# Kernel tuning notes

Hardware: AMD Instinct MI355X
Metric: run time of the kernel (lower is better)

The kernel has to match this reference:

```python
import jax, jax.numpy as jnp
import numpy as np

E, B, S, D, F = 8, 2, 1024, 1024, 4096


def setup_inputs() -> dict:
    key = jax.random.key(0)
    ks = jax.random.split(key, 9)
    sc_d = 1.0 / np.sqrt(D)
    sc_f = 1.0 / np.sqrt(F)
    hidden_states = jax.random.normal(ks[0], (B, S, D), dtype=jnp.float32)
    # router outputs set externally on the parent model in the original code
    gating_probs = jax.nn.softmax(jax.random.normal(ks[1], (B, E), dtype=jnp.float32), axis=-1)
    shared_gate_prob = jax.nn.sigmoid(jax.random.normal(ks[2], (B, 1), dtype=jnp.float32))
    # stacked expert SwiGLU MLP weights (Llama-style gate/up/down)
    Wg = jax.random.normal(ks[3], (E, D, F), dtype=jnp.float32) * sc_d
    Wu = jax.random.normal(ks[4], (E, D, F), dtype=jnp.float32) * sc_d
    Wd = jax.random.normal(ks[5], (E, F, D), dtype=jnp.float32) * sc_f
    # shared expert MLP
    Sg = jax.random.normal(ks[6], (D, F), dtype=jnp.float32) * sc_d
    Su = jax.random.normal(ks[7], (D, F), dtype=jnp.float32) * sc_d
    Sd = jax.random.normal(ks[8], (F, D), dtype=jnp.float32) * sc_f
    return {
        "hidden_states": hidden_states,
        "gating_probs": gating_probs,
        "shared_gate_prob": shared_gate_prob,
        "Wg": Wg, "Wu": Wu, "Wd": Wd,
        "Sg": Sg, "Su": Su, "Sd": Sd,
    }


def reference(hidden_states, gating_probs, shared_gate_prob, Wg, Wu, Wd, Sg, Su, Sd):
    h = hidden_states  # [B,S,D]
    # every expert's MLP runs on all tokens (naive all-experts-dense, as in source)
    g = jnp.einsum("bsd,edf->ebsf", h, Wg)
    u = jnp.einsum("bsd,edf->ebsf", h, Wu)
    expert_outs = jnp.einsum("ebsf,efd->ebsd", jax.nn.silu(g) * u, Wd)  # [E,B,S,D]
    # weighted_sum routing with per-sequence gating probs [B,E]
    expert_output = jnp.einsum("be,ebsd->bsd", gating_probs, expert_outs)
    # shared expert MLP
    shared = jnp.einsum("bsf,fd->bsd", jax.nn.silu(h @ Sg) * (h @ Su), Sd)
    sg = shared_gate_prob[:, :, None]  # [B,1,1]
    return (1.0 - sg) * expert_output + sg * shared
```

## Files before the change

kernel.cpp:

```cpp
#include <hip/hip_runtime.h>
#include <cstdio>
#include <cstdint>

typedef _Float16 f16;
typedef _Float16 f16x4 __attribute__((ext_vector_type(4)));
typedef _Float16 f16x8 __attribute__((ext_vector_type(8)));
typedef float f32x4 __attribute__((ext_vector_type(4)));

#define GLL16(gp, lp)                                                          \
  __builtin_amdgcn_global_load_lds(                                            \
      (const __attribute__((address_space(1))) void*)(gp),                     \
      (__attribute__((address_space(3))) void*)(lp), 16, 0, 0)

__global__ void cvt_f32_f16_kernel(const float* __restrict__ in,
                                   f16* __restrict__ out, int n4) {
  int i = blockIdx.x * blockDim.x + threadIdx.x;
  if (i < n4) {
    f32x4 v = reinterpret_cast<const f32x4*>(in)[i];
    f16x4 o;
    o[0] = (f16)v[0]; o[1] = (f16)v[1]; o[2] = (f16)v[2]; o[3] = (f16)v[3];
    reinterpret_cast<f16x4*>(out)[i] = o;
  }
}

__global__ void tr_cvt2_kernel(const float* __restrict__ inA,
                               const float* __restrict__ inB,
                               f16* __restrict__ out, size_t slotOff,
                               int C, size_t OS, int nA) {
  int slot = blockIdx.z;
  const float* src = (slot < nA) ? inA + (size_t)slot * 64 * gridDim.y * C : inB;
  f16* dst = out + (size_t)slot * slotOff;
  __shared__ f16 tl[4096];
  int t = threadIdx.x;
  int r0 = blockIdx.y * 64, c0 = blockIdx.x * 64;
  int br = (t >> 4) * 4, bc = (t & 15) * 4;
  f32x4 v[4];
#pragma unroll
  for (int i = 0; i < 4; ++i)
    v[i] = *(const f32x4*)&src[(size_t)(r0 + br + i) * C + c0 + bc];
#pragma unroll
  for (int cc = 0; cc < 4; ++cc) {
    int c = bc + cc;
    f16x4 o;
    o[0] = (f16)v[0][cc]; o[1] = (f16)v[1][cc];
    o[2] = (f16)v[2][cc]; o[3] = (f16)v[3][cc];
    *(f16x4*)&tl[c * 64 + (br ^ ((c & 7) * 8))] = o;
  }
  __syncthreads();
  int rw = (t & 7) * 8, cw = t >> 3;
#pragma unroll
  for (int j = 0; j < 2; ++j) {
    int c = cw + j * 32;
    f16x8 o = *(const f16x8*)&tl[c * 64 + (rw ^ ((c & 7) * 8))];
    *(f16x8*)&dst[(size_t)(c0 + c) * OS + r0 + rw] = o;
  }
}

#define BARX __builtin_amdgcn_s_barrier()
#define WAITV4 { asm volatile("s_waitcnt vmcnt(4)" ::: "memory"); __builtin_amdgcn_sched_barrier(0); }
#define WAITV0 { asm volatile("s_waitcnt vmcnt(0)" ::: "memory"); __builtin_amdgcn_sched_barrier(0); }
#define WAITL0 { asm volatile("s_waitcnt lgkmcnt(0)" ::: "memory"); __builtin_amdgcn_sched_barrier(0); }

#define STAGE_A(tile, hf)                                                      \
  do {                                                                         \
    const f16* g_ = Abase + (size_t)((hf) * 128) * LD + (tile) * 64 + aVoff;   \
    f16* d_ = &lds[(2 * ((tile) & 1) + (hf)) * 8192 + w * 512];                \
    GLL16(g_, d_);                                                             \
    GLL16(g_ + (size_t)64 * LD, d_ + 4096);                                    \
  } while (0)
#define STAGE_B(tile, hf)                                                      \
  do {                                                                         \
    const f16* g_ = Bbase + (size_t)((hf) * 128) * LD + (tile) * 64 + aVoff;   \
    f16* d_ = &lds[32768 + (2 * ((tile) & 1) + (hf)) * 8192 + w * 512];        \
    GLL16(g_, d_);                                                             \
    GLL16(g_ + (size_t)64 * LD, d_ + 4096);                                    \
  } while (0)

#define RD_A(rh, buf)                                                          \
  do {                                                                         \
    const f16* p_ = &lds[(2 * (buf) + wr) * 8192 + (rh) * 4096];               \
    aF[0][0] = *(const f16x8*)(p_ + 0 * 1024 + vR0);                           \
    aF[0][1] = *(const f16x8*)(p_ + 0 * 1024 + vR1);                           \
    aF[1][0] = *(const f16x8*)(p_ + 1 * 1024 + vR0);                           \
    aF[1][1] = *(const f16x8*)(p_ + 1 * 1024 + vR1);                           \
    aF[2][0] = *(const f16x8*)(p_ + 2 * 1024 + vR0);                           \
    aF[2][1] = *(const f16x8*)(p_ + 2 * 1024 + vR1);                           \
    aF[3][0] = *(const f16x8*)(p_ + 3 * 1024 + vR0);                           \
    aF[3][1] = *(const f16x8*)(p_ + 3 * 1024 + vR1);                           \
  } while (0)
#define RD_B(ch, buf)                                                          \
  do {                                                                         \
    const f16* p_ = &lds[32768 + (2 * (buf) + bh) * 8192 + bq * 4096 +         \
                         (ch) * 2 * 1024];                                     \
    bF[(ch) * 2][0] = *(const f16x8*)(p_ + vR0);                               \
    bF[(ch) * 2][1] = *(const f16x8*)(p_ + vR1);                               \
    bF[(ch) * 2 + 1][0] = *(const f16x8*)(p_ + 1024 + vR0);                    \
    bF[(ch) * 2 + 1][1] = *(const f16x8*)(p_ + 1024 + vR1);                    \
  } while (0)

#define MFMA16(rh, ch)                                                         \
  do {                                                                         \
    __builtin_amdgcn_s_setprio(1);                                             \
    _Pragma("unroll") for (int rt = 0; rt < 4; ++rt)                           \
        _Pragma("unroll") for (int ct = 0; ct < 2; ++ct)                       \
        _Pragma("unroll") for (int ks = 0; ks < 2; ++ks)                       \
            acc[(rh) * 4 + rt][(ch) * 2 + ct] =                                \
        __builtin_amdgcn_mfma_f32_16x16x32_f16(                                \
            aF[rt][ks], bF[(ch) * 2 + ct][ks], acc[(rh) * 4 + rt][(ch) * 2 + ct], \
            0, 0, 0);                                                          \
    __builtin_amdgcn_s_setprio(0);                                             \
    __builtin_amdgcn_sched_barrier(0);                                         \
  } while (0)

template <int MODE>
__global__ __launch_bounds__(512, 2) void gemm256_kernel(
    const f16* __restrict__ A, const f16* __restrict__ B, f16* __restrict__ T,
    float* __restrict__ P, const float* __restrict__ gate,
    const float* __restrict__ sgp) {
  constexpr size_t LD = (MODE == 2) ? 36864 : 1024;
  constexpr int NTILES = (MODE == 2) ? 72 : 16;
  __shared__ __align__(16) f16 lds[65536];

  int mt, nt, slot, kpart;
  if (MODE == 2) {
    int wg = (blockIdx.x & 7) * 32 + (blockIdx.x >> 3);
    kpart = wg >> 5; mt = (wg >> 2) & 7; nt = wg & 3; slot = 0;
  } else {
    int wg = ((blockIdx.x & 7) * 144) + (blockIdx.x >> 3);
    mt = wg / 144;
    int r144 = wg % 144;
    slot = r144 >> 4; nt = r144 & 15; kpart = 0;
  }

  int t = threadIdx.x, w = t >> 6, l = t & 63;
  int wr = w >> 2, wc = w & 3;
  int bh = wc >> 1, bq = wc & 1;

  int scol = (((l & 7) ^ ((l >> 3) & 7)) * 8);
  size_t stRow = (size_t)(w * 8 + (l >> 3)) * LD;
  size_t aVoff = stRow + scol;
  const f16* Abase;
  const f16* Bbase;
  if (MODE == 2) {
    Abase = A + (size_t)mt * 256 * LD + (size_t)kpart * 4608;
    Bbase = B + (size_t)nt * 256 * LD + (size_t)kpart * 4608;
  } else {
    Abase = A + (size_t)mt * 256 * LD;
    Bbase = B + (size_t)slot * 4096 * 1024 + (size_t)nt * 256 * LD;
  }

  int vR0 = (l & 15) * 64 + (((l >> 4) * 8) ^ ((l & 7) * 8));
  int vR1 = (l & 15) * 64 + ((32 + (l >> 4) * 8) ^ ((l & 7) * 8));

  f16x8 aF[4][2], bF[4][2];
  f32x4 acc[8][4] = {};

  STAGE_B(0, 0); STAGE_B(0, 1);
  STAGE_A(0, 0); STAGE_A(0, 1);
  STAGE_B(1, 0); STAGE_B(1, 1);
  WAITV4;
  BARX;

#pragma unroll 1
  for (int it = 0; it < NTILES / 2 - 1; ++it) {
    int t1 = 2 * it + 1, t2 = 2 * it + 2, t3 = 2 * it + 3;
    RD_A(0, 0); RD_B(0, 0); STAGE_A(t1, 0);
    BARX; WAITL0; MFMA16(0, 0); BARX;
    RD_B(1, 0); STAGE_A(t1, 1);
    BARX; WAITL0; MFMA16(0, 1); BARX;
    RD_A(1, 0); STAGE_B(t2, 0);
    BARX; WAITL0; MFMA16(1, 0); BARX;
    STAGE_B(t2, 1);
    BARX; MFMA16(1, 1); WAITV4; BARX;
    RD_A(0, 1); RD_B(0, 1); STAGE_A(t2, 0);
    BARX; WAITL0; MFMA16(0, 0); BARX;
    RD_B(1, 1); STAGE_A(t2, 1);
    BARX; WAITL0; MFMA16(0, 1); BARX;
    RD_A(1, 1); STAGE_B(t3, 0);
    BARX; WAITL0; MFMA16(1, 0); BARX;
    STAGE_B(t3, 1);
    BARX; MFMA16(1, 1); WAITV4; BARX;
  }
  RD_A(0, 0); RD_B(0, 0); STAGE_A(NTILES - 1, 0);
  BARX; WAITL0; MFMA16(0, 0); BARX;
  RD_B(1, 0); STAGE_A(NTILES - 1, 1);
  BARX; WAITL0; MFMA16(0, 1); BARX;
  RD_A(1, 0);
  BARX; WAITL0; MFMA16(1, 0); BARX;
  BARX; MFMA16(1, 1); WAITV0; BARX;
  RD_A(0, 1); RD_B(0, 1);
  BARX; WAITL0; MFMA16(0, 0); BARX;
  RD_B(1, 1);
  BARX; WAITL0; MFMA16(0, 1); BARX;
  RD_A(1, 1);
  BARX; WAITL0; MFMA16(1, 0); BARX;
  MFMA16(1, 1);

  int r0 = (l >> 4) * 4, c0 = l & 15;
  if (MODE == 2) {
    size_t base = ((size_t)kpart << 21);
    int rowbase = mt * 256 + wr * 128;
    int colbase = nt * 256 + wc * 64;
#pragma unroll
    for (int rt = 0; rt < 8; ++rt)
#pragma unroll
      for (int ct = 0; ct < 4; ++ct)
#pragma unroll
        for (int j = 0; j < 4; ++j)
          P[base + (size_t)(rowbase + rt * 16 + r0 + j) * 1024 + colbase +
            ct * 16 + c0] = acc[rt][ct][j];
  } else {
    int rowbase = mt * 256 + wr * 128;
    size_t colbase = (size_t)slot * 4096 + nt * 256 + wc * 64;
    float coef = 0.f;
    if (MODE == 1) {
      int b = mt >> 2;
      float s = sgp[b];
      coef = (slot < 8) ? (1.f - s) * gate[b * 8 + slot] : s;
    }
#pragma unroll
    for (int rt = 0; rt < 8; ++rt) {
#pragma unroll
      for (int ct = 0; ct < 4; ++ct) {
#pragma unroll
        for (int j = 0; j < 4; ++j) {
          size_t idx = (size_t)(rowbase + rt * 16 + r0 + j) * 36864 + colbase +
                       ct * 16 + c0;
          float v = acc[rt][ct][j];
          if (MODE == 0) {
            T[idx] = (f16)v;
          } else {
            float u = (float)T[idx];
            T[idx] = (f16)(v / (1.f + __expf(-v)) * u * coef);
          }
        }
      }
    }
  }
}

__global__ void reduce8_kernel(const float* __restrict__ P,
                               float* __restrict__ out, int n4) {
  int i = blockIdx.x * blockDim.x + threadIdx.x;
  if (i < n4) {
    f32x4 s = {0.f, 0.f, 0.f, 0.f};
#pragma unroll
    for (int e = 0; e < 8; ++e) {
      f32x4 v = reinterpret_cast<const f32x4*>(P + ((size_t)e << 21))[i];
      s += v;
    }
    reinterpret_cast<f32x4*>(out)[i] = s;
  }
}

extern "C" void kernel_launch(void* const* d_in, const int* in_sizes, int n_in,
                              void* d_out, int out_size, void* d_ws,
                              size_t ws_size, hipStream_t stream) {
  const float* h    = (const float*)d_in[0];
  const float* gate = (const float*)d_in[1];
  const float* sgp  = (const float*)d_in[2];
  const float* Wg   = (const float*)d_in[3];
  const float* Wu   = (const float*)d_in[4];
  const float* Wd   = (const float*)d_in[5];
  const float* Sg   = (const float*)d_in[6];
  const float* Su   = (const float*)d_in[7];
  const float* Sd   = (const float*)d_in[8];

  const size_t SZ_HB = 4194304;
  const size_t SZ_W  = 75497472;
  const size_t SZ_T  = 150994944;
  const size_t SZ_P  = 67108864;
  char* ws = (char*)d_ws;
  f16*   hb  = (f16*)(ws);
  f16*   WgT = (f16*)(ws + SZ_HB);
  f16*   WuT = (f16*)(ws + SZ_HB + SZ_W);
  f16*   WdT = (f16*)(ws + SZ_HB + 2 * SZ_W);
  f16*   T   = (f16*)(ws + SZ_HB + 3 * SZ_W);
  float* P   = (float*)(ws + SZ_HB + 3 * SZ_W + SZ_T);
  size_t need = SZ_HB + 3 * SZ_W + SZ_T + SZ_P;
  if (ws_size < need) {
    fprintf(stderr, "kernel_launch: ws too small (%zu < %zu)\n", ws_size, need);
    return;
  }
  float* out = (float*)d_out;

  cvt_f32_f16_kernel<<<2048, 256, 0, stream>>>(h, hb, 524288);
  tr_cvt2_kernel<<<dim3(64, 16, 9), 256, 0, stream>>>(
      Wg, Sg, WgT, 4096ull * 1024, 4096, 1024, 8);
  tr_cvt2_kernel<<<dim3(64, 16, 9), 256, 0, stream>>>(
      Wu, Su, WuT, 4096ull * 1024, 4096, 1024, 8);
  tr_cvt2_kernel<<<dim3(16, 64, 9), 256, 0, stream>>>(
      Wd, Sd, WdT, 4096, 1024, 36864, 8);

  gemm256_kernel<0><<<1152, 512, 0, stream>>>(hb, WuT, T, nullptr, nullptr, nullptr);
  gemm256_kernel<1><<<1152, 512, 0, stream>>>(hb, WgT, T, nullptr, gate, sgp);
  gemm256_kernel<2><<<256, 512, 0, stream>>>(T, WdT, nullptr, P, nullptr, nullptr);
  reduce8_kernel<<<2048, 256, 0, stream>>>(P, out, 524288);
}
```

Before: 651.6 us.

## Fuse gate and up projections into one dual-accumulator GEMM kernel

Replaces the two separate up and gate GEMM launches, which wrote the up result to T and then read it back in the gate epilogue, with a single kernel. It stages A once per K tile along with both Wg and Wu tiles (256x128 output tile) and keeps two accumulator sets, applying SiLU(g)*u*coef in the epilogue. This avoids re-reading A and the f16 round trip of T. The cost is smaller N tiles and double the accumulator registers, which may reduce occupancy or MFMA efficiency.

```diff
diff --git a/kernel.cpp b/kernel.cpp
--- a/kernel.cpp
+++ b/kernel.cpp
@@ -11,6 +11,11 @@
   __builtin_amdgcn_global_load_lds(                                            \
       (const __attribute__((address_space(1))) void*)(gp),                     \
       (__attribute__((address_space(3))) void*)(lp), 16, 0, 0)
+
+#define BARX __builtin_amdgcn_s_barrier()
+#define WAITV4 { asm volatile("s_waitcnt vmcnt(4)" ::: "memory"); __builtin_amdgcn_sched_barrier(0); }
+#define WAITV0 { asm volatile("s_waitcnt vmcnt(0)" ::: "memory"); __builtin_amdgcn_sched_barrier(0); }
+#define WAITL0 { asm volatile("s_waitcnt lgkmcnt(0)" ::: "memory"); __builtin_amdgcn_sched_barrier(0); }
 
 __global__ void cvt_f32_f16_kernel(const float* __restrict__ in,
                                    f16* __restrict__ out, int n4) {
@@ -56,10 +61,135 @@
   }
 }
 
-#define BARX __builtin_amdgcn_s_barrier()
-#define WAITV4 { asm volatile("s_waitcnt vmcnt(4)" ::: "memory"); __builtin_amdgcn_sched_barrier(0); }
-#define WAITV0 { asm volatile("s_waitcnt vmcnt(0)" ::: "memory"); __builtin_amdgcn_sched_barrier(0); }
-#define WAITL0 { asm volatile("s_waitcnt lgkmcnt(0)" ::: "memory"); __builtin_amdgcn_sched_barrier(0); }
+#define STAGE_A3(NB)                                                           \
+  do {                                                                         \
+    f16* d_ = &lds[(NB) * 16384 + ldsT];                                       \
+    GLL16(aS, d_); GLL16(aS + 65536, d_ + 4096);                               \
+    GLL16(aS + 131072, d_ + 8192); GLL16(aS + 196608, d_ + 12288);             \
+  } while (0)
+#define STAGE_G3(NB)                                                           \
+  do {                                                                         \
+    f16* d_ = &lds[32768 + (NB) * 16384 + ldsT];                               \
+    GLL16(gS, d_); GLL16(gS + 65536, d_ + 4096);                               \
+  } while (0)
+#define STAGE_U3(NB)                                                           \
+  do {                                                                         \
+    f16* d_ = &lds[32768 + (NB) * 16384 + 8192 + ldsT];                        \
+    GLL16(uS, d_); GLL16(uS + 65536, d_ + 4096);                               \
+  } while (0)
+
+#define RD3(BUF, VK)                                                           \
+  do {                                                                         \
+    const f16* pa_ = &lds[(BUF) * 16384 + wr * 4096 + vRow + (VK)];            \
+    aF[0] = *(const f16x8*)(pa_);                                              \
+    aF[1] = *(const f16x8*)(pa_ + 1024);                                       \
+    aF[2] = *(const f16x8*)(pa_ + 2048);                                       \
+    aF[3] = *(const f16x8*)(pa_ + 3072);                                       \
+    const f16* pg_ = &lds[32768 + (BUF) * 16384 + wc * 4096 + vRow + (VK)];    \
+    bG[0] = *(const f16x8*)(pg_);                                              \
+    bG[1] = *(const f16x8*)(pg_ + 1024);                                       \
+    bG[2] = *(const f16x8*)(pg_ + 2048);                                       \
+    bG[3] = *(const f16x8*)(pg_ + 3072);                                       \
+    const f16* pu_ = pg_ + 8192;                                               \
+    bU[0] = *(const f16x8*)(pu_);                                              \
+    bU[1] = *(const f16x8*)(pu_ + 1024);                                       \
+    bU[2] = *(const f16x8*)(pu_ + 2048);                                       \
+    bU[3] = *(const f16x8*)(pu_ + 3072);                                       \
+  } while (0)
+
+#define MFMA32()                                                               \
+  do {                                                                         \
+    __builtin_amdgcn_s_setprio(1);                                             \
+    _Pragma("unroll") for (int mi = 0; mi < 4; ++mi)                           \
+        _Pragma("unroll") for (int ni = 0; ni < 4; ++ni) {                     \
+      ag[mi][ni] = __builtin_amdgcn_mfma_f32_16x16x32_f16(aF[mi], bG[ni],      \
+                                                          ag[mi][ni], 0, 0, 0);\
+      au[mi][ni] = __builtin_amdgcn_mfma_f32_16x16x32_f16(aF[mi], bU[ni],      \
+                                                          au[mi][ni], 0, 0, 0);\
+    }                                                                          \
+    __builtin_amdgcn_s_setprio(0);                                             \
+    __builtin_amdgcn_sched_barrier(0);                                         \
+  } while (0)
+
+#define BODY3(BUF, DOSTA, DOSTB)                                               \
+  do {                                                                         \
+    RD3(BUF, vK0);                                                             \
+    if (DOSTA) { STAGE_A3((BUF) ^ 1); }                                        \
+    BARX; WAITL0;                                                              \
+    MFMA32();                                                                  \
+    BARX;                                                                      \
+    RD3(BUF, vK1);                                                             \
+    if (DOSTB) {                                                               \
+      STAGE_G3((BUF) ^ 1); STAGE_U3((BUF) ^ 1);                                \
+      aS += 64; gS += 64; uS += 64;                                            \
+    }                                                                          \
+    BARX; WAITL0;                                                              \
+    MFMA32();                                                                  \
+    if (DOSTB) { WAITV0; }                                                     \
+    BARX;                                                                      \
+  } while (0)
+
+__global__ __launch_bounds__(512, 2) void gemmUG3_kernel(
+    const f16* __restrict__ A, const f16* __restrict__ Bg,
+    const f16* __restrict__ Bu, f16* __restrict__ T,
+    const float* __restrict__ gate, const float* __restrict__ sgp) {
+  __shared__ __align__(16) f16 lds[65536];
+
+  int lgl = (blockIdx.x & 7) * 288 + (blockIdx.x >> 3);
+  int mt = lgl & 7;
+  int ntg = lgl >> 3;
+  int slot = ntg >> 5;
+
+  int t = threadIdx.x, w = t >> 6, l = t & 63;
+  int wr = w >> 1, wc = w & 1;
+
+  int kqs = (((t & 7) ^ ((t >> 3) & 7)) * 8);
+  const f16* aS = A + (size_t)(mt * 256 + (t >> 3)) * 1024 + kqs;
+  const f16* gS = Bg + (size_t)slot * 4194304 +
+                  (size_t)((ntg & 31) * 128 + (t >> 3)) * 1024 + kqs;
+  const f16* uS = Bu + (size_t)slot * 4194304 +
+                  (size_t)((ntg & 31) * 128 + (t >> 3)) * 1024 + kqs;
+  int ldsT = t * 8;
+
+  int vRow = (l & 15) * 64;
+  int vK0 = (((l >> 4) ^ (l & 7))) * 8;
+  int vK1 = (((4 + (l >> 4)) ^ (l & 7))) * 8;
+
+  f16x8 aF[4], bG[4], bU[4];
+  f32x4 ag[4][4] = {}, au[4][4] = {};
+
+  STAGE_A3(0); STAGE_G3(0); STAGE_U3(0);
+  aS += 64; gS += 64; uS += 64;
+  WAITV0; BARX;
+
+#pragma unroll 1
+  for (int it = 0; it < 7; ++it) {
+    BODY3(0, 1, 1);
+    BODY3(1, 1, 1);
+  }
+  BODY3(0, 1, 1);
+  BODY3(1, 0, 0);
+
+  int r0 = (l >> 4) * 4, c0 = l & 15;
+  int rowb = mt * 256 + wr * 64;
+  size_t colb = (size_t)ntg * 128 + wc * 64;
+  int b = mt >> 2;
+  float s = sgp[b];
+  float coef = (slot < 8) ? (1.f - s) * gate[b * 8 + slot] : s;
+#pragma unroll
+  for (int mi = 0; mi < 4; ++mi) {
+#pragma unroll
+    for (int ni = 0; ni < 4; ++ni) {
+#pragma unroll
+      for (int j = 0; j < 4; ++j) {
+        float g = ag[mi][ni][j];
+        float u = au[mi][ni][j];
+        T[(size_t)(rowb + mi * 16 + r0 + j) * 36864 + colb + ni * 16 + c0] =
+            (f16)(g / (1.f + __expf(-g)) * u * coef);
+      }
+    }
+  }
+}
 
 #define STAGE_A(tile, hf)                                                      \
   do {                                                                         \
@@ -79,23 +209,23 @@
 #define RD_A(rh, buf)                                                          \
   do {                                                                         \
     const f16* p_ = &lds[(2 * (buf) + wr) * 8192 + (rh) * 4096];               \
-    aF[0][0] = *(const f16x8*)(p_ + 0 * 1024 + vR0);                           \
-    aF[0][1] = *(const f16x8*)(p_ + 0 * 1024 + vR1);                           \
-    aF[1][0] = *(const f16x8*)(p_ + 1 * 1024 + vR0);                           \
-    aF[1][1] = *(const f16x8*)(p_ + 1 * 1024 + vR1);                           \
-    aF[2][0] = *(const f16x8*)(p_ + 2 * 1024 + vR0);                           \
-    aF[2][1] = *(const f16x8*)(p_ + 2 * 1024 + vR1);                           \
-    aF[3][0] = *(const f16x8*)(p_ + 3 * 1024 + vR0);                           \
-    aF[3][1] = *(const f16x8*)(p_ + 3 * 1024 + vR1);                           \
+    aFd[0][0] = *(const f16x8*)(p_ + 0 * 1024 + vR0);                          \
+    aFd[0][1] = *(const f16x8*)(p_ + 0 * 1024 + vR1);                          \
+    aFd[1][0] = *(const f16x8*)(p_ + 1 * 1024 + vR0);                          \
+    aFd[1][1] = *(const f16x8*)(p_ + 1 * 1024 + vR1);                          \
+    aFd[2][0] = *(const f16x8*)(p_ + 2 * 1024 + vR0);                          \
+    aFd[2][1] = *(const f16x8*)(p_ + 2 * 1024 + vR1);                          \
+    aFd[3][0] = *(const f16x8*)(p_ + 3 * 1024 + vR0);                          \
+    aFd[3][1] = *(const f16x8*)(p_ + 3 * 1024 + vR1);                          \
   } while (0)
 #define RD_B(ch, buf)                                                          \
   do {                                                                         \
     const f16* p_ = &lds[32768 + (2 * (buf) + bh) * 8192 + bq * 4096 +         \
                          (ch) * 2 * 1024];                                     \
-    bF[(ch) * 2][0] = *(const f16x8*)(p_ + vR0);                               \
-    bF[(ch) * 2][1] = *(const f16x8*)(p_ + vR1);                               \
-    bF[(ch) * 2 + 1][0] = *(const f16x8*)(p_ + 1024 + vR0);                    \
-    bF[(ch) * 2 + 1][1] = *(const f16x8*)(p_ + 1024 + vR1);                    \
+    bFd[(ch) * 2][0] = *(const f16x8*)(p_ + vR0);                              \
+    bFd[(ch) * 2][1] = *(const f16x8*)(p_ + vR1);                              \
+    bFd[(ch) * 2 + 1][0] = *(const f16x8*)(p_ + 1024 + vR0);                   \
+    bFd[(ch) * 2 + 1][1] = *(const f16x8*)(p_ + 1024 + vR1);                   \
   } while (0)
 
 #define MFMA16(rh, ch)                                                         \
@@ -106,31 +236,21 @@
         _Pragma("unroll") for (int ks = 0; ks < 2; ++ks)                       \
             acc[(rh) * 4 + rt][(ch) * 2 + ct] =                                \
         __builtin_amdgcn_mfma_f32_16x16x32_f16(                                \
-            aF[rt][ks], bF[(ch) * 2 + ct][ks], acc[(rh) * 4 + rt][(ch) * 2 + ct], \
-            0, 0, 0);                                                          \
+            aFd[rt][ks], bFd[(ch) * 2 + ct][ks],                               \
+            acc[(rh) * 4 + rt][(ch) * 2 + ct], 0, 0, 0);                       \
     __builtin_amdgcn_s_setprio(0);                                             \
     __builtin_amdgcn_sched_barrier(0);                                         \
   } while (0)
 
-template <int MODE>
-__global__ __launch_bounds__(512, 2) void gemm256_kernel(
-    const f16* __restrict__ A, const f16* __restrict__ B, f16* __restrict__ T,
-    float* __restrict__ P, const float* __restrict__ gate,
-    const float* __restrict__ sgp) {
-  constexpr size_t LD = (MODE == 2) ? 36864 : 1024;
-  constexpr int NTILES = (MODE == 2) ? 72 : 16;
+__global__ __launch_bounds__(512, 2) void gemmD_kernel(
+    const f16* __restrict__ A, const f16* __restrict__ B,
+    float* __restrict__ P) {
+  constexpr size_t LD = 36864;
+  constexpr int NTILES = 72;
   __shared__ __align__(16) f16 lds[65536];
 
-  int mt, nt, slot, kpart;
-  if (MODE == 2) {
-    int wg = (blockIdx.x & 7) * 32 + (blockIdx.x >> 3);
-    kpart = wg >> 5; mt = (wg >> 2) & 7; nt = wg & 3; slot = 0;
-  } else {
-    int wg = ((blockIdx.x & 7) * 144) + (blockIdx.x >> 3);
-    mt = wg / 144;
-    int r144 = wg % 144;
-    slot = r144 >> 4; nt = r144 & 15; kpart = 0;
-  }
+  int wg = (blockIdx.x & 7) * 32 + (blockIdx.x >> 3);
+  int kpart = wg >> 5, mt = (wg >> 2) & 7, nt = wg & 3;
 
   int t = threadIdx.x, w = t >> 6, l = t & 63;
   int wr = w >> 2, wc = w & 3;
@@ -139,20 +259,13 @@
   int scol = (((l & 7) ^ ((l >> 3) & 7)) * 8);
   size_t stRow = (size_t)(w * 8 + (l >> 3)) * LD;
   size_t aVoff = stRow + scol;
-  const f16* Abase;
-  const f16* Bbase;
-  if (MODE == 2) {
-    Abase = A + (size_t)mt * 256 * LD + (size_t)kpart * 4608;
-    Bbase = B + (size_t)nt * 256 * LD + (size_t)kpart * 4608;
-  } else {
-    Abase = A + (size_t)mt * 256 * LD;
-    Bbase = B + (size_t)slot * 4096 * 1024 + (size_t)nt * 256 * LD;
-  }
+  const f16* Abase = A + (size_t)mt * 256 * LD + (size_t)kpart * 4608;
+  const f16* Bbase = B + (size_t)nt * 256 * LD + (size_t)kpart * 4608;
 
   int vR0 = (l & 15) * 64 + (((l >> 4) * 8) ^ ((l & 7) * 8));
   int vR1 = (l & 15) * 64 + ((32 + (l >> 4) * 8) ^ ((l & 7) * 8));
 
-  f16x8 aF[4][2], bF[4][2];
+  f16x8 aFd[4][2], bFd[4][2];
   f32x4 acc[8][4] = {};
 
   STAGE_B(0, 0); STAGE_B(0, 1);
@@ -197,46 +310,17 @@
   MFMA16(1, 1);
 
   int r0 = (l >> 4) * 4, c0 = l & 15;
-  if (MODE == 2) {
-    size_t base = ((size_t)kpart << 21);
-    int rowbase = mt * 256 + wr * 128;
-    int colbase = nt * 256 + wc * 64;
-#pragma unroll
-    for (int rt = 0; rt < 8; ++rt)
-#pragma unroll
-      for (int ct = 0; ct < 4; ++ct)
-#pragma unroll
-        for (int j = 0; j < 4; ++j)
-          P[base + (size_t)(rowbase + rt * 16 + r0 + j) * 1024 + colbase +
-            ct * 16 + c0] = acc[rt][ct][j];
-  } else {
-    int rowbase = mt * 256 + wr * 128;
-    size_t colbase = (size_t)slot * 4096 + nt * 256 + wc * 64;
-    float coef = 0.f;
-    if (MODE == 1) {
-      int b = mt >> 2;
-      float s = sgp[b];
-      coef = (slot < 8) ? (1.f - s) * gate[b * 8 + slot] : s;
-    }
-#pragma unroll
-    for (int rt = 0; rt < 8; ++rt) {
-#pragma unroll
-      for (int ct = 0; ct < 4; ++ct) {
-#pragma unroll
-        for (int j = 0; j < 4; ++j) {
-          size_t idx = (size_t)(rowbase + rt * 16 + r0 + j) * 36864 + colbase +
-                       ct * 16 + c0;
-          float v = acc[rt][ct][j];
-          if (MODE == 0) {
-            T[idx] = (f16)v;
-          } else {
-            float u = (float)T[idx];
-            T[idx] = (f16)(v / (1.f + __expf(-v)) * u * coef);
-          }
-        }
-      }
-    }
-  }
+  size_t base = ((size_t)kpart << 21);
+  int rowbase = mt * 256 + wr * 128;
+  int colbase = nt * 256 + wc * 64;
+#pragma unroll
+  for (int rt = 0; rt < 8; ++rt)
+#pragma unroll
+    for (int ct = 0; ct < 4; ++ct)
+#pragma unroll
+      for (int j = 0; j < 4; ++j)
+        P[base + (size_t)(rowbase + rt * 16 + r0 + j) * 1024 + colbase +
+          ct * 16 + c0] = acc[rt][ct][j];
 }
 
 __global__ void reduce8_kernel(const float* __restrict__ P,
@@ -292,8 +376,7 @@
   tr_cvt2_kernel<<<dim3(16, 64, 9), 256, 0, stream>>>(
       Wd, Sd, WdT, 4096, 1024, 36864, 8);
 
-  gemm256_kernel<0><<<1152, 512, 0, stream>>>(hb, WuT, T, nullptr, nullptr, nullptr);
-  gemm256_kernel<1><<<1152, 512, 0, stream>>>(hb, WgT, T, nullptr, gate, sgp);
-  gemm256_kernel<2><<<256, 512, 0, stream>>>(T, WdT, nullptr, P, nullptr, nullptr);
+  gemmUG3_kernel<<<2304, 512, 0, stream>>>(hb, WgT, WuT, T, gate, sgp);
+  gemmD_kernel<<<256, 512, 0, stream>>>(T, WdT, P);
   reduce8_kernel<<<2048, 256, 0, stream>>>(P, out, 524288);
 }
```

New measurement: 576.6 us. 1.13x faster.
